# Kernel tuning notes

Hardware: AMD Instinct MI355X
Metric: run time of the kernel (lower is better)

The kernel has to match this reference:

```python
import jax, jax.numpy as jnp
import numpy as np

N_NODES = 100000
NEG_SLOPE = 0.2


def setup_inputs() -> dict:
    key = jax.random.key(0)
    k1, k2, k3, k4, k5 = jax.random.split(key, 5)
    N, E, Fin, Fout = N_NODES, 3200000, 128, 128
    x = jax.random.normal(k1, (N, Fin), dtype=jnp.float32)
    edge_index = jax.random.randint(k2, (2, E), 0, N, dtype=jnp.int64)
    # xavier-uniform for lin weight (fan_in=Fin, fan_out=Fout)
    limit = float(np.sqrt(6.0 / (Fin + Fout)))
    W = jax.random.uniform(k3, (Fin, Fout), jnp.float32, -limit, limit)
    # PyG glorot init for attention vectors (fan ~ Fout)
    alim = float(np.sqrt(6.0 / (1 + Fout)))
    att_src = jax.random.uniform(k4, (Fout,), jnp.float32, -alim, alim)
    att_dst = jax.random.uniform(k5, (Fout,), jnp.float32, -alim, alim)
    bias = jnp.zeros((Fout,), jnp.float32)
    return {"x": x, "edge_index": edge_index, "W": W,
            "att_src": att_src, "att_dst": att_dst, "bias": bias}


def reference(x, edge_index, W, att_src, att_dst, bias):
    N = x.shape[0]
    src, dst = edge_index[0], edge_index[1]  # messages flow src -> dst
    h = x @ W                                # [N, Fout]
    a_src = h @ att_src                      # [N]
    a_dst = h @ att_dst                      # [N]
    e = a_src[src] + a_dst[dst]              # [E]
    e = jax.nn.leaky_relu(e, NEG_SLOPE)
    # segment softmax over incoming edges of each dst node
    e_max = jax.ops.segment_max(e, dst, num_segments=N)  # [N]
    e_max = jnp.where(jnp.isfinite(e_max), e_max, 0.0)
    e_exp = jnp.exp(e - e_max[dst])          # [E]
    denom = jax.ops.segment_sum(e_exp, dst, num_segments=N)  # [N]
    alpha = e_exp / (denom[dst] + 1e-16)     # [E]
    # scatter-add weighted neighbor features
    out = jax.ops.segment_sum(alpha[:, None] * h[src], dst, num_segments=N)
    out = out + bias
    return jax.nn.relu(out)
```

## Files before the change

kernel.cpp:

```cpp
#include <hip/hip_runtime.h>
#include <cstdint>
#include <cstddef>

#define NEG 0.2f
#define CAP 10752
#define FINE_CAP CAP

typedef __attribute__((ext_vector_type(8))) short short8;
typedef __attribute__((ext_vector_type(4))) float f32x4;

__device__ __forceinline__ unsigned short f2bf(float f) {
  unsigned u = __float_as_uint(f);
  unsigned r = (u + 0x7fffu + ((u >> 16) & 1u)) >> 16;
  return (unsigned short)r;
}

__global__ __launch_bounds__(512) void k_detect(const int* __restrict__ ei32,
                                                int* __restrict__ flag,
                                                int* __restrict__ cursor,
                                                const float* __restrict__ W,
                                                unsigned short* __restrict__ Wt) {
  int t = threadIdx.x;
  cursor[t] = t * CAP;
  if (t < 64) {
    int v = ei32[2 * t + 1];
    unsigned long long b = __ballot(v != 0);
    if (t == 0) flag[0] = (b == 0ULL) ? 1 : 0;
  }
#pragma unroll
  for (int i = 0; i < 8; ++i) {
    int idx = i * 512 + t;
    float4 v = ((const float4*)W)[idx];
    int k = idx >> 5;
    int c = (idx & 31) * 4;
    Wt[(c + 0) * 128 + k] = f2bf(v.x);
    Wt[(c + 1) * 128 + k] = f2bf(v.y);
    Wt[(c + 2) * 128 + k] = f2bf(v.z);
    Wt[(c + 3) * 128 + k] = f2bf(v.w);
  }
}

__device__ __forceinline__ int edge_val(const void* ei, long long idx, int is64) {
  return is64 ? (int)((const long long*)ei)[idx] : ((const int*)ei)[idx];
}

#define MS_CHUNK 4096
__global__ __launch_bounds__(256) void k_fused(
    const float* __restrict__ x, const unsigned short* __restrict__ Wt,
    const float* __restrict__ as_, const float* __restrict__ ad_,
    unsigned short* __restrict__ hb, float* __restrict__ a_s,
    float* __restrict__ a_d, int N,
    const void* __restrict__ ei, const int* __restrict__ flag,
    int* __restrict__ cursor, uint32_t* __restrict__ buck, int E, int nms) {
  __shared__ int hist[512];
  __shared__ int resv[512];
  int gid = blockIdx.x;
  int t = threadIdx.x;
  bool is_ms = ((gid % 3) == 0) && ((gid / 3) < nms);

  if (is_ms) {
    int bid = gid / 3;
    const int is64 = flag[0];
    for (int i = t; i < 512; i += 256) hist[i] = 0;
    __syncthreads();
    long long base = (long long)bid * MS_CHUNK;
    uint32_t rec[16];
    int bb[16], rk[16];
#pragma unroll
    for (int i = 0; i < 16; ++i) {
      long long idx = base + i * 256 + t;
      bb[i] = -1;
      if (idx < E) {
        int s = edge_val(ei, idx, is64);
        int d = edge_val(ei, (long long)E + idx, is64);
        bb[i] = d >> 8;
        rec[i] = ((uint32_t)(d & 255) << 17) | (uint32_t)s;
        rk[i] = atomicAdd(&hist[bb[i]], 1);
      }
    }
    __syncthreads();
    for (int b = t; b < 512; b += 256) {
      int c = hist[b];
      resv[b] = c ? atomicAdd(&cursor[b], c) : 0;
    }
    __syncthreads();
#pragma unroll
    for (int i = 0; i < 16; ++i) {
      if (bb[i] >= 0) buck[(size_t)resv[bb[i]] + rk[i]] = rec[i];
    }
    return;
  }

  int gemm_id = gid - min(gid / 3 + 1, nms);
  int lane = t & 63;
  int wv = t >> 6;
  int row0 = gemm_id * 64 + wv * 16;
  int r = lane & 15, o = lane >> 4;

  int arow = row0 + r;
  if (arow >= N) arow = N - 1;
  const float* xr = x + (size_t)arow * 128 + o * 8;
  short8 a[4];
#pragma unroll
  for (int kt = 0; kt < 4; ++kt) {
    float4 lo = *(const float4*)(xr + kt * 32);
    float4 hi = *(const float4*)(xr + kt * 32 + 4);
    short8 av;
    av[0] = (short)f2bf(lo.x); av[1] = (short)f2bf(lo.y);
    av[2] = (short)f2bf(lo.z); av[3] = (short)f2bf(lo.w);
    av[4] = (short)f2bf(hi.x); av[5] = (short)f2bf(hi.y);
    av[6] = (short)f2bf(hi.z); av[7] = (short)f2bf(hi.w);
    a[kt] = av;
  }

  float ats[8], atd[8];
#pragma unroll
  for (int ct = 0; ct < 8; ++ct) {
    ats[ct] = as_[ct * 16 + r];
    atd[ct] = ad_[ct * 16 + r];
  }

  f32x4 acc[8];
#pragma unroll
  for (int ct = 0; ct < 8; ++ct) acc[ct] = (f32x4){0.f, 0.f, 0.f, 0.f};
#pragma unroll
  for (int ct = 0; ct < 8; ++ct) {
    const unsigned short* wb = Wt + ((size_t)(ct * 16 + r)) * 128 + o * 8;
#pragma unroll
    for (int kt = 0; kt < 4; ++kt) {
      short8 b = *(const short8*)(wb + kt * 32);
      acc[ct] = __builtin_amdgcn_mfma_f32_16x16x32_bf16(a[kt], b, acc[ct], 0, 0, 0);
    }
  }

#pragma unroll
  for (int j = 0; j < 4; ++j) {
    int row = row0 + o * 4 + j;
    bool ok = row < N;
    float ps = 0.f, pd = 0.f;
#pragma unroll
    for (int ct = 0; ct < 8; ++ct) {
      float v = acc[ct][j];
      if (ok) hb[(size_t)row * 128 + ct * 16 + r] = f2bf(v);
      ps += v * ats[ct];
      pd += v * atd[ct];
    }
#pragma unroll
    for (int d = 1; d <= 8; d <<= 1) {
      ps += __shfl_xor(ps, d);
      pd += __shfl_xor(pd, d);
    }
    if (ok && r == 0) { a_s[row] = ps; a_d[row] = pd; }
  }
}

__global__ __launch_bounds__(512) void k_bscan(const int* __restrict__ cursor,
                                               int* __restrict__ base,
                                               int NB, int E) {
  __shared__ int wsum[8];
  int t = threadIdx.x;
  int v = (t < NB) ? (cursor[t] - t * CAP) : 0;
  int lane = t & 63, w = t >> 6;
  int incl = v;
#pragma unroll
  for (int d = 1; d < 64; d <<= 1) {
    int o = __shfl_up(incl, d);
    if (lane >= d) incl += o;
  }
  if (lane == 63) wsum[w] = incl;
  __syncthreads();
  int woff = 0;
  for (int i = 0; i < w; ++i) woff += wsum[i];
  int excl = woff + incl - v;
  if (t < NB) base[t] = excl;
  if (t == 0) base[NB] = E;
}

__global__ __launch_bounds__(256) void k_fine(const int* __restrict__ base,
                                              const int* __restrict__ cursor,
                                              const uint32_t* __restrict__ buck,
                                              const float* __restrict__ a_s,
                                              const float* __restrict__ a_d,
                                              int* __restrict__ offsets,
                                              int* __restrict__ ssrc,
                                              float* __restrict__ wexp,
                                              int N, int E) {
  __shared__ int hist[256];
  __shared__ int cur[256];
  __shared__ int wsum[4];
  __shared__ float ad_sh[256];
  __shared__ uint32_t stage[FINE_CAP];
  int b = blockIdx.x;
  int t = threadIdx.x;
  int b0 = base[b];
  int cnt = cursor[b] - b * CAP;
  const uint32_t* bk = buck + (size_t)b * CAP;
  int node = (b << 8) + t;
  hist[t] = 0;
  ad_sh[t] = (node < N) ? a_d[node] : 0.f;
  __syncthreads();
  for (int i = t; i < cnt; i += 256) atomicAdd(&hist[bk[i] >> 17], 1);
  __syncthreads();
  int v = hist[t];
  int lane = t & 63, w = t >> 6;
  int incl = v;
#pragma unroll
  for (int d = 1; d < 64; d <<= 1) {
    int o = __shfl_up(incl, d);
    if (lane >= d) incl += o;
  }
  if (lane == 63) wsum[w] = incl;
  __syncthreads();
  int woff = 0;
  for (int i = 0; i < w; ++i) woff += wsum[i];
  int excl = woff + incl - v;
  cur[t] = excl;
  if (node < N) offsets[node] = b0 + excl;
  if (b == 0 && t == 0) offsets[N] = E;
  __syncthreads();
  for (int i = t; i < cnt; i += 256) {
    uint32_t r = bk[i];
    int pos = atomicAdd(&cur[r >> 17], 1);
    stage[pos] = r;
  }
  __syncthreads();
  for (int i = t; i < cnt; i += 256) {
    uint32_t r = stage[i];
    int s = (int)(r & 0x1ffffu);
    float e = a_s[s] + ad_sh[r >> 17];
    e = (e > 0.f) ? e : NEG * e;
    ssrc[b0 + i] = s;
    wexp[b0 + i] = __expf(e);
  }
}

#define AGG_LOAD(K, JJ)                                                   \
  {                                                                       \
    int e_ = ((JJ) * 4 + g) & 63;                                         \
    int ss_ = __shfl(s_l, e_);                                            \
    float ww_ = __shfl(w_l, e_);                                          \
    w##K = ((JJ) < iters) ? ww_ : 0.f;                                    \
    u##K = *(const uint4*)&hb[(size_t)ss_ * 128 + l16 * 8];               \
  }

#define AGG_FMA(K)                                                        \
  {                                                                       \
    acc[0] += w##K * __uint_as_float(u##K.x << 16);                       \
    acc[1] += w##K * __uint_as_float(u##K.x & 0xffff0000u);               \
    acc[2] += w##K * __uint_as_float(u##K.y << 16);                       \
    acc[3] += w##K * __uint_as_float(u##K.y & 0xffff0000u);               \
    acc[4] += w##K * __uint_as_float(u##K.z << 16);                       \
    acc[5] += w##K * __uint_as_float(u##K.z & 0xffff0000u);               \
    acc[6] += w##K * __uint_as_float(u##K.w << 16);                       \
    acc[7] += w##K * __uint_as_float(u##K.w & 0xffff0000u);               \
  }

__global__ __launch_bounds__(256) void k_agg(const int* __restrict__ offs,
                                             const int* __restrict__ ssrc,
                                             const float* __restrict__ wexp,
                                             const unsigned short* __restrict__ hb,
                                             const float* __restrict__ bias,
                                             float* __restrict__ out, int N) {
  int lane = threadIdx.x & 63;
  int n = blockIdx.x * 4 + (threadIdx.x >> 6);
  if (n >= N) return;
  int g = lane >> 4;
  int l16 = lane & 15;
  float acc[8] = {};
  float sum = 0.f;
  int s0 = offs[n], s1 = offs[n + 1];

  for (int base = s0; base < s1; base += 64) {
    int idx = base + lane;
    int s_l = 0;
    float w_l = 0.f;
    if (idx < s1) {
      s_l = ssrc[idx];
      w_l = wexp[idx];
    }
    sum += w_l;
    int cnt = min(64, s1 - base);
    int iters = (cnt + 3) >> 2;
    uint4 u0, u1, u2, u3;
    float w0, w1, w2, w3;
    AGG_LOAD(0, 0) AGG_LOAD(1, 1) AGG_LOAD(2, 2) AGG_LOAD(3, 3)
    int j = 0;
    for (; j + 4 < iters; j += 4) {
      AGG_FMA(0) AGG_LOAD(0, j + 4)
      AGG_FMA(1) AGG_LOAD(1, j + 5)
      AGG_FMA(2) AGG_LOAD(2, j + 6)
      AGG_FMA(3) AGG_LOAD(3, j + 7)
    }
    AGG_FMA(0) AGG_FMA(1) AGG_FMA(2) AGG_FMA(3)
  }
#pragma unroll
  for (int d = 1; d <= 32; d <<= 1) sum += __shfl_xor(sum, d);
#pragma unroll
  for (int d = 16; d <= 32; d <<= 1) {
#pragma unroll
    for (int i = 0; i < 8; ++i) acc[i] += __shfl_xor(acc[i], d);
  }
  float inv = 1.0f / (sum + 1e-16f);
  if (lane < 32) {
    int half = g & 1;
    int f = l16 * 8 + half * 4;
    float4 bv = *(const float4*)&bias[f];
    float4 o;
    o.x = fmaxf(acc[half * 4 + 0] * inv + bv.x, 0.f);
    o.y = fmaxf(acc[half * 4 + 1] * inv + bv.y, 0.f);
    o.z = fmaxf(acc[half * 4 + 2] * inv + bv.z, 0.f);
    o.w = fmaxf(acc[half * 4 + 3] * inv + bv.w, 0.f);
    *(float4*)&out[(size_t)n * 128 + f] = o;
  }
}

extern "C" void kernel_launch(void* const* d_in, const int* in_sizes, int n_in,
                              void* d_out, int out_size, void* d_ws, size_t ws_size,
                              hipStream_t stream) {
  const float* x = (const float*)d_in[0];
  const void* ei = d_in[1];
  const float* W = (const float*)d_in[2];
  const float* att_s = (const float*)d_in[3];
  const float* att_d = (const float*)d_in[4];
  const float* bias = (const float*)d_in[5];
  float* out = (float*)d_out;

  const int N = in_sizes[0] / 128;
  const int E = in_sizes[1] / 2;
  const int NB = (N + 255) >> 8;

  uint8_t* ws = (uint8_t*)d_ws;
  size_t off = 0;
  auto alloc = [&](size_t bytes) -> void* {
    void* p = ws + off;
    off = (off + bytes + 511) & ~(size_t)511;
    return p;
  };
  int* flag = (int*)alloc(4);
  int* bcur = (int*)alloc(512 * 4);
  int* bbase = (int*)alloc(513 * 4);
  unsigned short* Wt = (unsigned short*)alloc(128 * 128 * 2);
  int* offsets = (int*)alloc((size_t)(N + 1) * 4);
  int* ssrc = (int*)alloc((size_t)E * 4);
  float* wexp = (float*)alloc((size_t)E * 4);
  unsigned short* hb = (unsigned short*)alloc((size_t)N * 128 * 2);
  float* a_s = (float*)alloc((size_t)N * 4);
  float* a_d = (float*)alloc((size_t)N * 4);
  uint32_t* buck = (uint32_t*)d_out;
  (void)ws_size; (void)n_in; (void)out_size;

  const int ngemm = (N + 63) / 64;
  const int nms = (E + MS_CHUNK - 1) / MS_CHUNK;
  int grid = ngemm + nms;
  if (grid < 3 * nms - 2) grid = 3 * nms - 2;

  k_detect<<<1, 512, 0, stream>>>((const int*)ei, flag, bcur, W, Wt);
  k_fused<<<grid, 256, 0, stream>>>(x, Wt, att_s, att_d, hb, a_s, a_d, N,
                                    ei, flag, bcur, buck, E, nms);
  k_bscan<<<1, 512, 0, stream>>>(bcur, bbase, NB, E);
  k_fine<<<NB, 256, 0, stream>>>(bbase, bcur, buck, a_s, a_d, offsets, ssrc, wexp, N, E);
  k_agg<<<(N + 3) / 4, 256, 0, stream>>>(offsets, ssrc, wexp, hb, bias, out, N);
}
```

Measured before the change: 207.9 us.

## Interleave edge src/weight, widen k_fine blocks, deepen aggregation prefetch

Packs each edge's source index and exp weight into a single int2 array, so the fine-sort kernel does one 8-byte store and the aggregation kernel one 8-byte load per edge instead of two separate streams. k_fine now runs 1024 threads per block, with only the first 256 doing the histogram scan work, to put more threads on the bucket scatter and weight computation. The aggregation loop keeps 8 gathered rows in flight instead of 4, hiding more gather latency. The extra in-flight registers may lower occupancy, and nodes with few edges waste more of the fixed unrolled loads.

```diff
diff --git a/kernel.cpp b/kernel.cpp
--- a/kernel.cpp
+++ b/kernel.cpp
@@ -176,15 +176,14 @@
   if (t == 0) base[NB] = E;
 }
 
-__global__ __launch_bounds__(256) void k_fine(const int* __restrict__ base,
-                                              const int* __restrict__ cursor,
-                                              const uint32_t* __restrict__ buck,
-                                              const float* __restrict__ a_s,
-                                              const float* __restrict__ a_d,
-                                              int* __restrict__ offsets,
-                                              int* __restrict__ ssrc,
-                                              float* __restrict__ wexp,
-                                              int N, int E) {
+__global__ __launch_bounds__(1024) void k_fine(const int* __restrict__ base,
+                                               const int* __restrict__ cursor,
+                                               const uint32_t* __restrict__ buck,
+                                               const float* __restrict__ a_s,
+                                               const float* __restrict__ a_d,
+                                               int* __restrict__ offsets,
+                                               int2* __restrict__ sw,
+                                               int N, int E) {
   __shared__ int hist[256];
   __shared__ int cur[256];
   __shared__ int wsum[4];
@@ -195,42 +194,48 @@
   int b0 = base[b];
   int cnt = cursor[b] - b * CAP;
   const uint32_t* bk = buck + (size_t)b * CAP;
-  int node = (b << 8) + t;
-  hist[t] = 0;
-  ad_sh[t] = (node < N) ? a_d[node] : 0.f;
-  __syncthreads();
-  for (int i = t; i < cnt; i += 256) atomicAdd(&hist[bk[i] >> 17], 1);
-  __syncthreads();
-  int v = hist[t];
-  int lane = t & 63, w = t >> 6;
-  int incl = v;
-#pragma unroll
-  for (int d = 1; d < 64; d <<= 1) {
-    int o = __shfl_up(incl, d);
-    if (lane >= d) incl += o;
-  }
-  if (lane == 63) wsum[w] = incl;
-  __syncthreads();
-  int woff = 0;
-  for (int i = 0; i < w; ++i) woff += wsum[i];
-  int excl = woff + incl - v;
-  cur[t] = excl;
-  if (node < N) offsets[node] = b0 + excl;
+  int node = (b << 8) + (t & 255);
+  if (t < 256) {
+    hist[t] = 0;
+    ad_sh[t] = (node < N) ? a_d[node] : 0.f;
+  }
+  __syncthreads();
+  for (int i = t; i < cnt; i += 1024) atomicAdd(&hist[bk[i] >> 17], 1);
+  __syncthreads();
+  int v = 0, incl = 0;
+  int lane = t & 63, w4 = t >> 6;
+  if (t < 256) {
+    v = hist[t];
+    incl = v;
+#pragma unroll
+    for (int d = 1; d < 64; d <<= 1) {
+      int o = __shfl_up(incl, d);
+      if (lane >= d) incl += o;
+    }
+    if (lane == 63) wsum[w4] = incl;
+  }
+  __syncthreads();
+  if (t < 256) {
+    int woff = 0;
+    for (int i = 0; i < w4; ++i) woff += wsum[i];
+    int excl = woff + incl - v;
+    cur[t] = excl;
+    if (node < N) offsets[node] = b0 + excl;
+  }
   if (b == 0 && t == 0) offsets[N] = E;
   __syncthreads();
-  for (int i = t; i < cnt; i += 256) {
+  for (int i = t; i < cnt; i += 1024) {
     uint32_t r = bk[i];
     int pos = atomicAdd(&cur[r >> 17], 1);
     stage[pos] = r;
   }
   __syncthreads();
-  for (int i = t; i < cnt; i += 256) {
+  for (int i = t; i < cnt; i += 1024) {
     uint32_t r = stage[i];
     int s = (int)(r & 0x1ffffu);
     float e = a_s[s] + ad_sh[r >> 17];
     e = (e > 0.f) ? e : NEG * e;
-    ssrc[b0 + i] = s;
-    wexp[b0 + i] = __expf(e);
+    sw[b0 + i] = make_int2(s, __float_as_int(__expf(e)));
   }
 }
 
@@ -256,8 +261,7 @@
   }
 
 __global__ __launch_bounds__(256) void k_agg(const int* __restrict__ offs,
-                                             const int* __restrict__ ssrc,
-                                             const float* __restrict__ wexp,
+                                             const int2* __restrict__ sw,
                                              const unsigned short* __restrict__ hb,
                                              const float* __restrict__ bias,
                                              float* __restrict__ out, int N) {
@@ -275,23 +279,30 @@
     int s_l = 0;
     float w_l = 0.f;
     if (idx < s1) {
-      s_l = ssrc[idx];
-      w_l = wexp[idx];
+      int2 m = sw[idx];
+      s_l = m.x;
+      w_l = __int_as_float(m.y);
     }
     sum += w_l;
     int cnt = min(64, s1 - base);
     int iters = (cnt + 3) >> 2;
-    uint4 u0, u1, u2, u3;
-    float w0, w1, w2, w3;
+    uint4 u0, u1, u2, u3, u4, u5, u6, u7;
+    float w0, w1, w2, w3, w4, w5, w6, w7;
     AGG_LOAD(0, 0) AGG_LOAD(1, 1) AGG_LOAD(2, 2) AGG_LOAD(3, 3)
+    AGG_LOAD(4, 4) AGG_LOAD(5, 5) AGG_LOAD(6, 6) AGG_LOAD(7, 7)
     int j = 0;
-    for (; j + 4 < iters; j += 4) {
-      AGG_FMA(0) AGG_LOAD(0, j + 4)
-      AGG_FMA(1) AGG_LOAD(1, j + 5)
-      AGG_FMA(2) AGG_LOAD(2, j + 6)
-      AGG_FMA(3) AGG_LOAD(3, j + 7)
+    for (; j + 8 < iters; j += 8) {
+      AGG_FMA(0) AGG_LOAD(0, j + 8)
+      AGG_FMA(1) AGG_LOAD(1, j + 9)
+      AGG_FMA(2) AGG_LOAD(2, j + 10)
+      AGG_FMA(3) AGG_LOAD(3, j + 11)
+      AGG_FMA(4) AGG_LOAD(4, j + 12)
+      AGG_FMA(5) AGG_LOAD(5, j + 13)
+      AGG_FMA(6) AGG_LOAD(6, j + 14)
+      AGG_FMA(7) AGG_LOAD(7, j + 15)
     }
     AGG_FMA(0) AGG_FMA(1) AGG_FMA(2) AGG_FMA(3)
+    AGG_FMA(4) AGG_FMA(5) AGG_FMA(6) AGG_FMA(7)
   }
 #pragma unroll
   for (int d = 1; d <= 32; d <<= 1) sum += __shfl_xor(sum, d);
@@ -341,8 +352,7 @@
   int* bbase = (int*)alloc(513 * 4);
   unsigned short* Wt = (unsigned short*)alloc(128 * 128 * 2);
   int* offsets = (int*)alloc((size_t)(N + 1) * 4);
-  int* ssrc = (int*)alloc((size_t)E * 4);
-  float* wexp = (float*)alloc((size_t)E * 4);
+  int2* sw = (int2*)alloc((size_t)E * 8);
   unsigned short* hb = (unsigned short*)alloc((size_t)N * 128 * 2);
   float* a_s = (float*)alloc((size_t)N * 4);
   float* a_d = (float*)alloc((size_t)N * 4);
@@ -358,6 +368,6 @@
   k_fused<<<grid, 256, 0, stream>>>(x, Wt, att_s, att_d, hb, a_s, a_d, N,
                                     ei, flag, bcur, buck, E, nms);
   k_bscan<<<1, 512, 0, stream>>>(bcur, bbase, NB, E);
-  k_fine<<<NB, 256, 0, stream>>>(bbase, bcur, buck, a_s, a_d, offsets, ssrc, wexp, N, E);
-  k_agg<<<(N + 3) / 4, 256, 0, stream>>>(offsets, ssrc, wexp, hb, bias, out, N);
-}
+  k_fine<<<NB, 1024, 0, stream>>>(bbase, bcur, buck, a_s, a_d, offsets, sw, N, E);
+  k_agg<<<(N + 3) / 4, 256, 0, stream>>>(offsets, sw, hb, bias, out, N);
+}
```

After: 224.5 us. +8.0%, slower.
